# Kernel optimization log

Hardware: AMD Instinct MI355X
Metric: run time of the kernel (lower is better)

Reference implementation:

```python
import jax, jax.numpy as jnp
import numpy as np

# Hardware-emulation constants (from init_kwargs, NeuroSim-style QLinear)
WL_IN = 8        # input activation bit width (bit-serial)
WL_W = 8         # weight bit width
CELL_BIT = 2     # bits per memory cell -> 4 weight slices
SUB = 128        # crossbar sub-array size (rows summed in analog)
ADC_BITS = 5     # ADC precision per partial sum
ONOFF = 10.0     # cell on/off conductance ratio
VARI = 0.05      # multiplicative device variation sigma


def _adc_quant(x, bits, axes):
    # LinearQuantizeOut: uniform quantization between tensor min/max
    mn = jnp.min(x, axis=axes, keepdims=True)
    mx = jnp.max(x, axis=axes, keepdims=True)
    step = (mx - mn) * (2.0 ** (-bits))
    step = jnp.where(step <= 0, 1.0, step)
    idx = jnp.clip(jnp.floor((x - mn) / step), 0.0, 2.0 ** bits - 1.0)
    return idx * step + mn


def _qlinear_hw(x, w, noise):
    """Analog PIM crossbar emulation of y = x @ w.T with bit-serial inputs,
    bit-sliced cells, on/off-ratio offset + dummy column, device variation,
    per-subarray ADC quantization."""
    B, N = x.shape
    F = w.shape[0]
    I, W, K = WL_IN, WL_W, WL_W // CELL_BIT
    cr = 2.0 ** CELL_BIT
    lower, upper = 1.0 / ONOFF, 1.0
    S = (N + SUB - 1) // SUB
    Np = S * SUB
    # quantize input to I bits in [0,1]; weight to W-bit integer in [0, 2^W-1]
    xq = jnp.round(jnp.clip(x, 0.0, 1.0) * (2.0 ** I - 1.0))            # [B, N]
    Xi = jnp.clip(jnp.round((w + 1.0) * 0.5 * (2.0 ** W - 1.0)), 0.0, 2.0 ** W - 1.0)  # [F, N]
    xq = jnp.pad(xq, ((0, 0), (0, Np - N)))
    Xi = jnp.pad(Xi, ((0, 0), (0, Np - N)))
    zpow = 2.0 ** jnp.arange(I, dtype=x.dtype)
    kpow = cr ** jnp.arange(K, dtype=x.dtype)
    bits = jnp.mod(jnp.floor(xq[..., None] / zpow), 2.0)                # [B, Np, I]
    slc = jnp.mod(jnp.floor(Xi[..., None] / kpow), cr)                  # [F, Np, K]
    g = slc * (upper - lower) + (cr - 1.0) * lower                      # cell conductances
    g = g * (1.0 + VARI * noise)                                        # device variation
    bits = bits.reshape(B, S, SUB, I)
    g = g.reshape(F, S, SUB, K)
    # analog partial sums per (input bit i, subarray s, weight slice k)
    P = jnp.einsum('bsai,fsak->iskbf', bits, g)                         # [I,S,K,B,F]
    # dummy column (all cells at lowest conductance), identical across F
    D = jnp.transpose(bits.sum(axis=2), (2, 1, 0)) * ((cr - 1.0) * lower)  # [I,S,B]
    Pq = _adc_quant(P, ADC_BITS, axes=(3, 4))
    Dq = _adc_quant(D, ADC_BITS, axes=(2,))
    scal = (2.0 ** jnp.arange(I, dtype=x.dtype))[:, None] * (cr ** jnp.arange(K, dtype=x.dtype))[None, :]
    acc = jnp.einsum('iskbf,ik->bf', Pq - Dq[:, :, None, :, None], scal) / (upper - lower)
    # undo integer mappings: w = 2*Xi/(2^W-1) - 1, x = xq/(2^I-1)
    out = 2.0 * acc / ((2.0 ** I - 1.0) * (2.0 ** W - 1.0)) \
          - xq.sum(axis=1, keepdims=True) / (2.0 ** I - 1.0)
    return out


def _qlinear(x, w, noise):
    # straight-through quantized weight (WAGE-style STE) + hardware forward
    Xi = jnp.clip(jnp.round((w + 1.0) * 0.5 * (2.0 ** WL_W - 1.0)), 0.0, 2.0 ** WL_W - 1.0)
    wq = 2.0 * Xi / (2.0 ** WL_W - 1.0) - 1.0
    wq_ste = w + jax.lax.stop_gradient(wq - w)
    out_ideal = x @ wq_ste.T
    out_hw = _qlinear_hw(x, w, noise)
    return out_ideal + jax.lax.stop_gradient(out_hw - out_ideal)


def setup_inputs() -> dict:
    key = jax.random.key(0)
    k1, k2, k3, k4, k5 = jax.random.split(key, 5)
    x = jax.random.uniform(k1, (1024, 784), dtype=jnp.float32)
    w1 = jax.random.normal(k2, (512, 784), dtype=jnp.float32) * 0.05
    w3 = jax.random.normal(k3, (10, 512), dtype=jnp.float32) * 0.08
    noise1 = jax.random.normal(k4, (512, 896, 4), dtype=jnp.float32)  # 784 padded to 7*128
    noise3 = jax.random.normal(k5, (10, 512, 4), dtype=jnp.float32)   # 512 = 4*128 exact
    return {"x": x, "w1": w1, "w3": w3, "noise1": noise1, "noise3": noise3}


def reference(x, w1, w3, noise1, noise3):
    h = jnp.tanh(_qlinear(x, w1, noise1))   # QLinear(784,512) + Tanh
    return _qlinear(h, w3, noise3)          # QLinear(512,10)
```

## Files before the change

kernel.cpp:

```cpp
#include <hip/hip_runtime.h>

#define FLTMAX 3.402823466e+38f


__device__ __forceinline__ void grid_barrier(unsigned* bar, int s, unsigned nblk)
{
    __syncthreads();
    if (threadIdx.x == 0) {
        unsigned* ctr = bar + s * 128;
        unsigned* rel = bar + 896 + s * 16;
        asm volatile("s_waitcnt vmcnt(0)" ::: "memory");
        __hip_atomic_fetch_add(&ctr[(blockIdx.x & 7) << 4], 1u,
                               __ATOMIC_RELAXED, __HIP_MEMORY_SCOPE_AGENT);
        if (blockIdx.x == 0) {
            for (int it = 0; it < (1 << 20); ++it) {
                unsigned tot = 0;
#pragma unroll
                for (int j = 0; j < 8; ++j)
                    tot += __hip_atomic_load(&ctr[j << 4], __ATOMIC_RELAXED,
                                             __HIP_MEMORY_SCOPE_AGENT);
                if (tot >= nblk) break;
                __builtin_amdgcn_s_sleep(8);
            }
            __hip_atomic_store(rel, 1u, __ATOMIC_RELAXED, __HIP_MEMORY_SCOPE_AGENT);
        } else {
            for (int it = 0; it < (1 << 20); ++it) {
                if (__hip_atomic_load(rel, __ATOMIC_RELAXED,
                                      __HIP_MEMORY_SCOPE_AGENT) != 0u)
                    break;
                __builtin_amdgcn_s_sleep(16);
            }
        }
    }
    __syncthreads();
}

__global__ void prep1_kernel(const float* __restrict__ x, float* __restrict__ sx1,
                             unsigned* __restrict__ xqbT, unsigned* __restrict__ stats1,
                             unsigned* __restrict__ bar)
{
    __shared__ float xr[896];
    __shared__ float red[128];
    int b = blockIdx.x;
    if (b == 0) {
        for (int t = threadIdx.x; t < 224; t += 128) {
            stats1[t * 2] = 0x7F7FFFFFu; stats1[t * 2 + 1] = 0u;
        }
        for (int t = threadIdx.x; t < 1008; t += 128) bar[t] = 0u;
    }
    float psum = 0.f;
    for (int n = threadIdx.x; n < 896; n += 128) {
        float v = 0.f;
        if (n < 784) {
            float xv = x[b * 784 + n];
            xv = fminf(fmaxf(xv, 0.f), 1.f);
            v = rintf(__fmul_rn(xv, 255.f));
        }
        xr[n] = v;
        psum += v;
    }
    red[threadIdx.x] = psum;
    __syncthreads();
    for (int w = 64; w >= 1; w >>= 1) {
        if (threadIdx.x < w) red[threadIdx.x] += red[threadIdx.x + w];
        __syncthreads();
    }
    if (threadIdx.x == 0) sx1[b] = red[0];
    if (threadIdx.x < 28) {
        int w = threadIdx.x;
        unsigned words[8] = {0, 0, 0, 0, 0, 0, 0, 0};
#pragma unroll 8
        for (int n = 0; n < 32; ++n) {
            int v = (int)xr[w * 32 + n];
#pragma unroll
            for (int i = 0; i < 8; ++i) words[i] |= ((unsigned)((v >> i) & 1)) << n;
        }
#pragma unroll
        for (int i = 0; i < 8; ++i) xqbT[(i * 28 + w) * 1024 + b] = words[i];
    }
}

__global__ void prepg1t_kernel(const float* __restrict__ w1, const float* __restrict__ noise1,
                               float* __restrict__ g1t)
{
    __shared__ float t[4][32][33];
    const int n0 = blockIdx.x * 32, f0 = blockIdx.y * 32;
    const int tid = threadIdx.x;
    {
        int n = tid & 31, fi = tid >> 5;
#pragma unroll
        for (int p = 0; p < 4; ++p) {
            int f = p * 8 + fi;
            int gn = n0 + n, gf = f0 + f;
            float gv[4] = {0.f, 0.f, 0.f, 0.f};
            if (gn < 784) {
                float w = w1[gf * 784 + gn];
                float Xi = fminf(fmaxf(rintf(__fmul_rn(__fmul_rn(__fadd_rn(w, 1.f), 0.5f), 255.f)),
                                       0.f), 255.f);
                int xi = (int)Xi;
                float4 nz = *(const float4*)&noise1[(gf * 896 + gn) * 4];
                float nzv[4] = {nz.x, nz.y, nz.z, nz.w};
#pragma unroll
                for (int k = 0; k < 4; ++k) {
                    int slc = (xi >> (2 * k)) & 3;
                    float base = __fadd_rn(__fmul_rn((float)slc, 0.9f), 0.3f);
                    float nf = __fadd_rn(1.f, __fmul_rn(0.05f, nzv[k]));
                    gv[k] = __fmul_rn(base, nf);
                }
            }
#pragma unroll
            for (int k = 0; k < 4; ++k) t[k][n][f] = gv[k];
        }
    }
    __syncthreads();
    {
        int f = tid & 31, nn = tid >> 5;
#pragma unroll
        for (int p = 0; p < 4; ++p) {
            int n = p * 8 + nn;
#pragma unroll
            for (int k = 0; k < 4; ++k)
                g1t[(n0 + n) * 2048 + k * 512 + f0 + f] = t[k][n][f];
        }
    }
}

__global__ void prepg2_kernel(const float* __restrict__ w3, const float* __restrict__ noise3,
                              float* __restrict__ g2t)
{
    int gid = blockIdx.x * 256 + threadIdx.x;
    if (gid >= 10 * 512) return;
    int f = gid / 512, n = gid % 512;
    float w = w3[f * 512 + n];
    float Xi = fminf(fmaxf(rintf(__fmul_rn(__fmul_rn(__fadd_rn(w, 1.f), 0.5f), 255.f)),
                           0.f), 255.f);
    int xi = (int)Xi;
#pragma unroll
    for (int k = 0; k < 4; ++k) {
        int slc = (xi >> (2 * k)) & 3;
        float base = __fadd_rn(__fmul_rn((float)slc, 0.9f), 0.3f);
        float nf = __fadd_rn(1.f, __fmul_rn(0.05f, noise3[(f * 512 + n) * 4 + k]));
        g2t[n * 40 + k * 10 + f] = __fmul_rn(base, nf);
    }
}

__global__ void dqpopT_kernel(const unsigned* __restrict__ xqbT, float* __restrict__ Dq)
{
    __shared__ float red[512];
    const int i = blockIdx.x / 7, s = blockIdx.x % 7;
    const int tid = threadIdx.x;
    float D[4];
    float mn = FLTMAX, mx = -FLTMAX;
#pragma unroll
    for (int u = 0; u < 4; ++u) {
        int b = tid + u * 256;
        int c = 0;
#pragma unroll
        for (int w = 0; w < 4; ++w)
            c += __popc(xqbT[(i * 28 + s * 4 + w) * 1024 + b]);
        D[u] = __fmul_rn((float)c, 0.3f);
        mn = fminf(mn, D[u]);
        mx = fmaxf(mx, D[u]);
    }
    red[tid] = mn; red[256 + tid] = mx;
    __syncthreads();
    for (int w = 128; w >= 1; w >>= 1) {
        if (tid < w) {
            red[tid] = fminf(red[tid], red[tid + w]);
            red[256 + tid] = fmaxf(red[256 + tid], red[256 + tid + w]);
        }
        __syncthreads();
    }
    mn = red[0]; mx = red[256];
    float step = __fmul_rn(__fsub_rn(mx, mn), 0.03125f);
    if (step <= 0.f) step = 1.f;
#pragma unroll
    for (int u = 0; u < 4; ++u) {
        int b = tid + u * 256;
        float idx = fminf(fmaxf(floorf(__fdiv_rn(__fsub_rn(D[u], mn), step)), 0.f), 31.f);
        Dq[(i * 7 + s) * 1024 + b] = __fadd_rn(__fmul_rn(idx, step), mn);
    }
}

__global__ void dqpop_kernel(const unsigned* __restrict__ xqb, float* __restrict__ Dq,
                             int S, int wpr)
{
    __shared__ float red[512];
    const int i = blockIdx.x / S, s = blockIdx.x % S;
    const int tid = threadIdx.x;
    float D[4];
    float mn = FLTMAX, mx = -FLTMAX;
#pragma unroll
    for (int u = 0; u < 4; ++u) {
        int b = tid + u * 256;
        uint4 w = *(const uint4*)&xqb[(i * 1024 + b) * wpr + s * 4];
        int c = __popc(w.x) + __popc(w.y) + __popc(w.z) + __popc(w.w);
        D[u] = __fmul_rn((float)c, 0.3f);
        mn = fminf(mn, D[u]);
        mx = fmaxf(mx, D[u]);
    }
    red[tid] = mn; red[256 + tid] = mx;
    __syncthreads();
    for (int w = 128; w >= 1; w >>= 1) {
        if (tid < w) {
            red[tid] = fminf(red[tid], red[tid + w]);
            red[256 + tid] = fmaxf(red[256 + tid], red[256 + tid + w]);
        }
        __syncthreads();
    }
    mn = red[0]; mx = red[256];
    float step = __fmul_rn(__fsub_rn(mx, mn), 0.03125f);
    if (step <= 0.f) step = 1.f;
#pragma unroll
    for (int u = 0; u < 4; ++u) {
        int b = tid + u * 256;
        float idx = fminf(fmaxf(floorf(__fdiv_rn(__fsub_rn(D[u], mn), step)), 0.f), 31.f);
        Dq[(i * S + s) * 1024 + b] = __fadd_rn(__fmul_rn(idx, step), mn);
    }
}

#define BK 32
__global__ __launch_bounds__(256, 4) void mm1_kernel(
    const unsigned* __restrict__ xqbT, const float* __restrict__ g1t,
    unsigned char* __restrict__ Pidx, unsigned* stats, unsigned* bar)
{
    __shared__ __align__(16) float Bs[BK][132];
    __shared__ unsigned Abits[128];
    __shared__ float red[512];
    __shared__ __align__(16) unsigned stage[128 * 33];
    const int tid = threadIdx.x;
    const int r = blockIdx.x & 63;
    const int i = r >> 3;
    const int btile = r & 7;
    const int b0 = btile * 128;
    const int colgrp = blockIdx.x >> 6;
    const int colBase = colgrp * 128;
    const int tx = tid & 15, ty = tid >> 4;
    const int aB = tid >> 5;
    const int eB = (tid & 31) << 2;
    const int k = colgrp >> 2;
    const int wv = tid >> 6, ln = tid & 63;
    const int rsub = ln >> 3, chunk = ln & 7;

    for (int s = 0; s < 7; ++s) {
        float4 pB[4];
        unsigned pAw = 0;
#pragma unroll
        for (int u = 0; u < 4; ++u)
            pB[u] = *(const float4*)&g1t[(s * 128 + u * 8 + aB) * 2048 + colBase + eB];
        if (tid < 128) pAw = xqbT[(i * 28 + s * 4) * 1024 + b0 + tid];

        float acc[8][8] = {};

        for (int ac = 0; ac < 4; ++ac) {
            __syncthreads();
#pragma unroll
            for (int u = 0; u < 4; ++u)
                *(float4*)&Bs[u * 8 + aB][eB] = pB[u];
            if (tid < 128) Abits[tid] = pAw;
            __syncthreads();

            if (ac < 3) {
                const int n0 = s * 128 + (ac + 1) * BK;
#pragma unroll
                for (int u = 0; u < 4; ++u)
                    pB[u] = *(const float4*)&g1t[(n0 + u * 8 + aB) * 2048 + colBase + eB];
                if (tid < 128) pAw = xqbT[(i * 28 + s * 4 + ac + 1) * 1024 + b0 + tid];
            }

            unsigned wrd[8];
#pragma unroll
            for (int u = 0; u < 4; ++u) {
                wrd[u]     = Abits[(ty << 2) + u];
                wrd[4 + u] = Abits[64 + (ty << 2) + u];
            }

#pragma unroll 4
            for (int a = 0; a < BK; ++a) {
                float br[8];
                *(float4*)&br[0] = *(const float4*)&Bs[a][(tx << 2)];
                *(float4*)&br[4] = *(const float4*)&Bs[a][64 + (tx << 2)];
#pragma unroll
                for (int u = 0; u < 8; ++u) {
                    float ab = (float)((wrd[u] >> a) & 1u);
#pragma unroll
                    for (int v = 0; v < 8; ++v)
                        acc[u][v] = fmaf(ab, br[v], acc[u][v]);
                }
            }
        }

        float mn = acc[0][0], mx = acc[0][0];
#pragma unroll
        for (int u = 0; u < 8; ++u)
#pragma unroll
            for (int v = 0; v < 8; ++v) { mn = fminf(mn, acc[u][v]); mx = fmaxf(mx, acc[u][v]); }
        red[tid] = mn; red[256 + tid] = mx;
        __syncthreads();
        for (int w = 128; w >= 1; w >>= 1) {
            if (tid < w) {
                red[tid] = fminf(red[tid], red[tid + w]);
                red[256 + tid] = fmaxf(red[256 + tid], red[256 + tid + w]);
            }
            __syncthreads();
        }
        const int slot = ((s * 8 + i) * 4 + k) * 2;
        if (tid == 0) {
            atomicMin(&stats[slot], __float_as_uint(red[0]));
            atomicMax(&stats[slot + 1], __float_as_uint(red[256]));
        }

        grid_barrier(bar, s, 1024u);

        unsigned mnu = __hip_atomic_load(&stats[slot],     __ATOMIC_RELAXED,
                                         __HIP_MEMORY_SCOPE_AGENT);
        unsigned mxu = __hip_atomic_load(&stats[slot + 1], __ATOMIC_RELAXED,
                                         __HIP_MEMORY_SCOPE_AGENT);
        float qmn = __uint_as_float(mnu);
        float qmx = __uint_as_float(mxu);
        float step = __fmul_rn(__fsub_rn(qmx, qmn), 0.03125f);
        if (step <= 0.f) step = 1.f;

#pragma unroll
        for (int uh = 0; uh < 2; ++uh)
#pragma unroll
            for (int u = 0; u < 4; ++u) {
                int rr = uh * 64 + (ty << 2) + u;
#pragma unroll
                for (int vh = 0; vh < 2; ++vh) {
                    float ix;
                    unsigned pack;
                    ix = fminf(fmaxf(floorf(__fdiv_rn(__fsub_rn(acc[uh * 4 + u][vh * 4 + 0], qmn), step)), 0.f), 31.f);
                    pack = (unsigned)(int)ix;
                    ix = fminf(fmaxf(floorf(__fdiv_rn(__fsub_rn(acc[uh * 4 + u][vh * 4 + 1], qmn), step)), 0.f), 31.f);
                    pack |= (unsigned)(int)ix << 8;
                    ix = fminf(fmaxf(floorf(__fdiv_rn(__fsub_rn(acc[uh * 4 + u][vh * 4 + 2], qmn), step)), 0.f), 31.f);
                    pack |= (unsigned)(int)ix << 16;
                    ix = fminf(fmaxf(floorf(__fdiv_rn(__fsub_rn(acc[uh * 4 + u][vh * 4 + 3], qmn), step)), 0.f), 31.f);
                    pack |= (unsigned)(int)ix << 24;
                    stage[rr * 33 + vh * 16 + tx] = pack;
                }
            }
        __syncthreads();

        unsigned char* tbase = Pidx +
            ((size_t)(((s * 8 + i) * 16 + colgrp) * 8 + btile)) * 16384;
#pragma unroll
        for (int t = 0; t < 4; ++t) {
            int rr = t * 32 + wv * 8 + rsub;
            const unsigned* sp = &stage[rr * 33 + chunk * 4];
            uint4 v = make_uint4(sp[0], sp[1], sp[2], sp[3]);
            *(uint4*)&tbase[rr * 128 + chunk * 16] = v;
        }
    }
}

__global__ void fold1_kernel(const unsigned char* __restrict__ Pidx,
                             const unsigned* __restrict__ stats,
                             const float* __restrict__ Dq1, const float* __restrict__ sx1,
                             float* __restrict__ xq2, unsigned* __restrict__ xqb2,
                             float* __restrict__ sx2)
{
    __shared__ float red[512];
    __shared__ float dt;
    __shared__ float2 st[224];
    int b = blockIdx.x;
    int f = threadIdx.x;
    if (f < 224) {
        float mn = __uint_as_float(stats[f * 2]);
        float mx = __uint_as_float(stats[f * 2 + 1]);
        float step = __fmul_rn(__fsub_rn(mx, mn), 0.03125f);
        if (step <= 0.f) step = 1.f;
        st[f] = make_float2(mn, step);
    }
    if (f == 0) {
        float sd = 0.f;
        for (int i = 0; i < 8; ++i) {
            float sc = (float)(85 << i);
            for (int ss = 0; ss < 7; ++ss) sd = fmaf(Dq1[(i * 7 + ss) * 1024 + b], sc, sd);
        }
        dt = sd;
    }
    __syncthreads();
    const int fhi = f >> 7, fl = f & 127;
    const unsigned char* pb = Pidx + (size_t)(b >> 7) * 16384
                                   + (size_t)(b & 127) * 128 + fl;
    float accR = 0.f;
    for (int s = 0; s < 7; ++s) {
        float sum = 0.f;
        for (int i = 0; i < 8; ++i) {
            const int si16 = (s * 8 + i) * 16;
#pragma unroll
            for (int kk = 0; kk < 4; ++kk) {
                float2 ms = st[((s * 8 + i) << 2) + kk];
                float ixv = (float)pb[(size_t)(si16 + kk * 4 + fhi) * 131072];
                float pq = __fadd_rn(__fmul_rn(ixv, ms.y), ms.x);
                sum = fmaf(pq, (float)(1 << (i + 2 * kk)), sum);
            }
        }
        accR = __fadd_rn(accR, sum);
    }
    float total = __fsub_rn(accR, dt);
    float acc = __fdiv_rn(total, 0.9f);
    float o = __fsub_rn(__fdiv_rn(__fmul_rn(2.f, acc), 65025.f), __fdiv_rn(sx1[b], 255.f));
    float h = tanhf(o);
    h = fminf(fmaxf(h, 0.f), 1.f);
    float code = rintf(__fmul_rn(h, 255.f));
    xq2[b * 512 + f] = code;
    int ci = (int)code;
    int lane = f & 63;
#pragma unroll
    for (int i = 0; i < 8; ++i) {
        unsigned long long m = __ballot((ci >> i) & 1);
        if ((lane & 31) == 0) {
            unsigned wv = (lane & 32) ? (unsigned)(m >> 32) : (unsigned)m;
            xqb2[(i * 1024 + b) * 16 + (f >> 5)] = wv;
        }
    }
    red[f] = code;
    __syncthreads();
    for (int w = 256; w >= 1; w >>= 1) {
        if (f < w) red[f] += red[f + w];
        __syncthreads();
    }
    if (f == 0) sx2[b] = red[0];
}

__global__ void mm2_kernel(const float* __restrict__ xq2, const float* __restrict__ g2t,
                           float* __restrict__ P2)
{
    int gid = blockIdx.x * 256 + threadIdx.x;
    if (gid >= 40960) return;
    int f = gid % 10;
    int b = (gid / 10) & 1023;
    int s = gid / 10240;
    float acc[8][4] = {};
    for (int a = 0; a < 128; ++a) {
        int n = s * 128 + a;
        int xi = (int)xq2[b * 512 + n];
        float g0 = g2t[n * 40 + f];
        float gA = g2t[n * 40 + 10 + f];
        float gB = g2t[n * 40 + 20 + f];
        float gC = g2t[n * 40 + 30 + f];
#pragma unroll
        for (int i = 0; i < 8; ++i) {
            float bi = (float)((xi >> i) & 1);
            acc[i][0] = fmaf(bi, g0, acc[i][0]);
            acc[i][1] = fmaf(bi, gA, acc[i][1]);
            acc[i][2] = fmaf(bi, gB, acc[i][2]);
            acc[i][3] = fmaf(bi, gC, acc[i][3]);
        }
    }
#pragma unroll
    for (int i = 0; i < 8; ++i)
#pragma unroll
        for (int k = 0; k < 4; ++k)
            P2[(size_t)((s * 8 + i) * 4 + k) * 10240 + b * 10 + f] = acc[i][k];
}

__global__ void stat2_kernel(const float* __restrict__ P2, float2* __restrict__ stats2)
{
    __shared__ float red[512];
    int p = blockIdx.x;
    int tid = threadIdx.x;
    float mn = FLTMAX, mx = -FLTMAX;
    for (int t = tid; t < 10240; t += 256) {
        float v = P2[(size_t)p * 10240 + t];
        mn = fminf(mn, v); mx = fmaxf(mx, v);
    }
    red[tid] = mn; red[256 + tid] = mx;
    __syncthreads();
    for (int w = 128; w >= 1; w >>= 1) {
        if (tid < w) {
            red[tid] = fminf(red[tid], red[tid + w]);
            red[256 + tid] = fmaxf(red[256 + tid], red[256 + tid + w]);
        }
        __syncthreads();
    }
    if (tid == 0) {
        float step = __fmul_rn(__fsub_rn(red[256], red[0]), 0.03125f);
        if (step <= 0.f) step = 1.f;
        stats2[p] = make_float2(red[0], step);
    }
}

__global__ void out2_kernel(const float* __restrict__ P2, const float2* __restrict__ stats2,
                            const float* __restrict__ Dq2, const float* __restrict__ sx2,
                            float* __restrict__ out)
{
    int gid = blockIdx.x * 256 + threadIdx.x;
    if (gid >= 10240) return;
    int b = gid / 10;
    float dt = 0.f;
    for (int i = 0; i < 8; ++i) {
        float sc = (float)(85 << i);
        for (int s = 0; s < 4; ++s) dt = fmaf(Dq2[(i * 4 + s) * 1024 + b], sc, dt);
    }
    float sum = 0.f;
    for (int s = 0; s < 4; ++s)
        for (int i = 0; i < 8; ++i)
#pragma unroll
            for (int k = 0; k < 4; ++k) {
                int p = (s * 8 + i) * 4 + k;
                float2 st = stats2[p];
                float val = P2[(size_t)p * 10240 + gid];
                float idx = fminf(fmaxf(floorf(__fdiv_rn(__fsub_rn(val, st.x), st.y)), 0.f), 31.f);
                float pq = __fadd_rn(__fmul_rn(idx, st.y), st.x);
                sum = fmaf(pq, (float)(1 << (i + 2 * k)), sum);
            }
    float total = __fsub_rn(sum, dt);
    float acc = __fdiv_rn(total, 0.9f);
    out[gid] = __fsub_rn(__fdiv_rn(__fmul_rn(2.f, acc), 65025.f), __fdiv_rn(sx2[b], 255.f));
}

extern "C" void kernel_launch(void* const* d_in, const int* in_sizes, int n_in,
                              void* d_out, int out_size, void* d_ws, size_t ws_size,
                              hipStream_t stream)
{
    const float* x      = (const float*)d_in[0];
    const float* w1     = (const float*)d_in[1];
    const float* w3     = (const float*)d_in[2];
    const float* noise1 = (const float*)d_in[3];
    const float* noise3 = (const float*)d_in[4];
    float* out = (float*)d_out;
    float* ws  = (float*)d_ws;

    float*         g1t    = ws + 0;
    float*         xq2    = ws + 1835008;
    float*         P2     = ws + 2359296;
    float*         g2t    = ws + 3670016;
    float*         Dq1    = ws + 3690496;
    float*         Dq2    = ws + 3747840;
    float*         sx1    = ws + 3780608;
    float*         sx2    = ws + 3781632;
    float2*        stats2 = (float2*)(ws + 3782656);
    unsigned*      stats1 = (unsigned*)(ws + 3782912);
    unsigned*      xqbT   = (unsigned*)(ws + 3783424);
    unsigned*      xqb2   = (unsigned*)(ws + 4012800);
    unsigned char* Pidx   = (unsigned char*)(ws + 4143872);
    unsigned*      bar    = (unsigned*)(ws + 33504256);

    prep1_kernel<<<1024, 128, 0, stream>>>(x, sx1, xqbT, stats1, bar);
    prepg1t_kernel<<<dim3(28, 16), 256, 0, stream>>>(w1, noise1, g1t);
    dqpopT_kernel<<<56, 256, 0, stream>>>(xqbT, Dq1);

    mm1_kernel<<<1024, 256, 0, stream>>>(xqbT, g1t, Pidx, stats1, bar);

    fold1_kernel<<<1024, 512, 0, stream>>>(Pidx, stats1, Dq1, sx1, xq2, xqb2, sx2);
    prepg2_kernel<<<20, 256, 0, stream>>>(w3, noise3, g2t);
    dqpop_kernel<<<32, 256, 0, stream>>>(xqb2, Dq2, 4, 16);
    mm2_kernel<<<160, 256, 0, stream>>>(xq2, g2t, P2);
    stat2_kernel<<<128, 256, 0, stream>>>(P2, stats2);
    out2_kernel<<<40, 256, 0, stream>>>(P2, stats2, Dq2, sx2, out);
}
```

Before: 666.7 us.

## Replace whole-grid barrier with per-stats-slot barrier and wave-shuffle reduction

Each (s,i,k) partial-sum group now synchronizes only the 32 blocks that share its ADC min/max slot, using a per-slot counter, instead of waiting on a barrier across all 1024 blocks at every subarray step. The block-level min/max reduction switches from a shared-memory tree with many __syncthreads to wave shuffles plus a 4-entry combine. The staged byte-output write is re-indexed so consecutive threads write consecutive 16B chunks, and a trailing sync is added. The barrier area grows to 3584 words. Correctness still depends on all 32 blocks of a slot being co-resident.

```diff
diff --git a/kernel.cpp b/kernel.cpp
--- a/kernel.cpp
+++ b/kernel.cpp
@@ -3,33 +3,16 @@
 #define FLTMAX 3.402823466e+38f
 
 
-__device__ __forceinline__ void grid_barrier(unsigned* bar, int s, unsigned nblk)
+__device__ __forceinline__ void slot_barrier(unsigned* ctr, unsigned target)
 {
     __syncthreads();
     if (threadIdx.x == 0) {
-        unsigned* ctr = bar + s * 128;
-        unsigned* rel = bar + 896 + s * 16;
         asm volatile("s_waitcnt vmcnt(0)" ::: "memory");
-        __hip_atomic_fetch_add(&ctr[(blockIdx.x & 7) << 4], 1u,
-                               __ATOMIC_RELAXED, __HIP_MEMORY_SCOPE_AGENT);
-        if (blockIdx.x == 0) {
-            for (int it = 0; it < (1 << 20); ++it) {
-                unsigned tot = 0;
-#pragma unroll
-                for (int j = 0; j < 8; ++j)
-                    tot += __hip_atomic_load(&ctr[j << 4], __ATOMIC_RELAXED,
-                                             __HIP_MEMORY_SCOPE_AGENT);
-                if (tot >= nblk) break;
-                __builtin_amdgcn_s_sleep(8);
-            }
-            __hip_atomic_store(rel, 1u, __ATOMIC_RELAXED, __HIP_MEMORY_SCOPE_AGENT);
-        } else {
-            for (int it = 0; it < (1 << 20); ++it) {
-                if (__hip_atomic_load(rel, __ATOMIC_RELAXED,
-                                      __HIP_MEMORY_SCOPE_AGENT) != 0u)
-                    break;
-                __builtin_amdgcn_s_sleep(16);
-            }
+        __hip_atomic_fetch_add(ctr, 1u, __ATOMIC_RELAXED, __HIP_MEMORY_SCOPE_AGENT);
+        for (int it = 0; it < (1 << 22); ++it) {
+            if (__hip_atomic_load(ctr, __ATOMIC_RELAXED, __HIP_MEMORY_SCOPE_AGENT) >= target)
+                break;
+            __builtin_amdgcn_s_sleep(2);
         }
     }
     __syncthreads();
@@ -46,7 +29,7 @@
         for (int t = threadIdx.x; t < 224; t += 128) {
             stats1[t * 2] = 0x7F7FFFFFu; stats1[t * 2 + 1] = 0u;
         }
-        for (int t = threadIdx.x; t < 1008; t += 128) bar[t] = 0u;
+        for (int t = threadIdx.x; t < 3584; t += 128) bar[t] = 0u;
     }
     float psum = 0.f;
     for (int n = threadIdx.x; n < 896; n += 128) {
@@ -220,13 +203,15 @@
 }
 
 #define BK 32
-__global__ __launch_bounds__(256, 4) void mm1_kernel(
+__global__ __launch_bounds__(256)
+__attribute__((amdgpu_waves_per_eu(4, 4)))
+void mm1_kernel(
     const unsigned* __restrict__ xqbT, const float* __restrict__ g1t,
     unsigned char* __restrict__ Pidx, unsigned* stats, unsigned* bar)
 {
     __shared__ __align__(16) float Bs[BK][132];
     __shared__ unsigned Abits[128];
-    __shared__ float red[512];
+    __shared__ float redmn[4], redmx[4];
     __shared__ __align__(16) unsigned stage[128 * 33];
     const int tid = threadIdx.x;
     const int r = blockIdx.x & 63;
@@ -240,7 +225,6 @@
     const int eB = (tid & 31) << 2;
     const int k = colgrp >> 2;
     const int wv = tid >> 6, ln = tid & 63;
-    const int rsub = ln >> 3, chunk = ln & 7;
 
     for (int s = 0; s < 7; ++s) {
         float4 pB[4];
@@ -294,27 +278,29 @@
 #pragma unroll
         for (int u = 0; u < 8; ++u)
 #pragma unroll
-            for (int v = 0; v < 8; ++v) { mn = fminf(mn, acc[u][v]); mx = fmaxf(mx, acc[u][v]); }
-        red[tid] = mn; red[256 + tid] = mx;
-        __syncthreads();
-        for (int w = 128; w >= 1; w >>= 1) {
-            if (tid < w) {
-                red[tid] = fminf(red[tid], red[tid + w]);
-                red[256 + tid] = fmaxf(red[256 + tid], red[256 + tid + w]);
-            }
-            __syncthreads();
-        }
-        const int slot = ((s * 8 + i) * 4 + k) * 2;
+            for (int v = 0; v < 8; ++v) {
+                mn = fminf(mn, acc[u][v]); mx = fmaxf(mx, acc[u][v]);
+            }
+#pragma unroll
+        for (int o = 32; o >= 1; o >>= 1) {
+            mn = fminf(mn, __shfl_xor(mn, o));
+            mx = fmaxf(mx, __shfl_xor(mx, o));
+        }
+        if (ln == 0) { redmn[wv] = mn; redmx[wv] = mx; }
+        __syncthreads();
+        const int slot = ((s * 8 + i) * 4 + k);
         if (tid == 0) {
-            atomicMin(&stats[slot], __float_as_uint(red[0]));
-            atomicMax(&stats[slot + 1], __float_as_uint(red[256]));
-        }
-
-        grid_barrier(bar, s, 1024u);
-
-        unsigned mnu = __hip_atomic_load(&stats[slot],     __ATOMIC_RELAXED,
+            float m0 = fminf(fminf(redmn[0], redmn[1]), fminf(redmn[2], redmn[3]));
+            float m1 = fmaxf(fmaxf(redmx[0], redmx[1]), fmaxf(redmx[2], redmx[3]));
+            atomicMin(&stats[slot * 2],     __float_as_uint(m0));
+            atomicMax(&stats[slot * 2 + 1], __float_as_uint(m1));
+        }
+
+        slot_barrier(&bar[slot * 16], 32u);
+
+        unsigned mnu = __hip_atomic_load(&stats[slot * 2],     __ATOMIC_RELAXED,
                                          __HIP_MEMORY_SCOPE_AGENT);
-        unsigned mxu = __hip_atomic_load(&stats[slot + 1], __ATOMIC_RELAXED,
+        unsigned mxu = __hip_atomic_load(&stats[slot * 2 + 1], __ATOMIC_RELAXED,
                                          __HIP_MEMORY_SCOPE_AGENT);
         float qmn = __uint_as_float(mnu);
         float qmx = __uint_as_float(mxu);
@@ -343,15 +329,19 @@
             }
         __syncthreads();
 
-        unsigned char* tbase = Pidx +
-            ((size_t)(((s * 8 + i) * 16 + colgrp) * 8 + btile)) * 16384;
-#pragma unroll
-        for (int t = 0; t < 4; ++t) {
-            int rr = t * 32 + wv * 8 + rsub;
-            const unsigned* sp = &stage[rr * 33 + chunk * 4];
-            uint4 v = make_uint4(sp[0], sp[1], sp[2], sp[3]);
-            *(uint4*)&tbase[rr * 128 + chunk * 16] = v;
-        }
+        {
+            unsigned char* tbase = Pidx +
+                ((size_t)(((s * 8 + i) * 16 + colgrp) * 8 + btile)) * 16384;
+#pragma unroll
+            for (int rep = 0; rep < 4; ++rep) {
+                int j = rep * 256 + tid;
+                int rr = j >> 3, c4 = (j & 7) << 2;
+                const unsigned* sp = &stage[rr * 33 + c4];
+                uint4 v = make_uint4(sp[0], sp[1], sp[2], sp[3]);
+                *(uint4*)&tbase[(size_t)j * 16] = v;
+            }
+        }
+        __syncthreads();
     }
 }
 
```

Result: slower. 681.8 us (+2.3%).
